# Optimization experiments

Measured on AMD Instinct MI355X. Metric: run time of the kernel, lower is better.

## Reference

```python
import jax, jax.numpy as jnp
import numpy as np

S = 4096
F = 512  # in_features, head_num == 1 so per-head dim == F


def setup_inputs() -> dict:
    key = jax.random.key(0)
    ks = jax.random.split(key, 11)
    std = 0.02
    inp = {
        "q": jax.random.normal(ks[0], (1, S, F), jnp.float32),
        "k": jax.random.normal(ks[1], (1, S, F), jnp.float32),
        "v": jax.random.normal(ks[2], (1, S, F), jnp.float32),
        "Wq": jax.random.normal(ks[3], (F, F), jnp.float32) * std,
        "bq": jax.random.normal(ks[4], (F,), jnp.float32) * std,
        "Wk": jax.random.normal(ks[5], (F, F), jnp.float32) * std,
        "bk": jax.random.normal(ks[6], (F,), jnp.float32) * std,
        "Wv": jax.random.normal(ks[7], (F, F), jnp.float32) * std,
        "bv": jax.random.normal(ks[8], (F,), jnp.float32) * std,
        "Wo": jax.random.normal(ks[9], (F, F), jnp.float32) * std,
        "bo": jax.random.normal(ks[10], (F,), jnp.float32) * std,
    }
    return inp


def reference(q, k, v, Wq, bq, Wk, bk, Wv, bv, Wo, bo):
    dk = Wq.shape[0]  # head_num == 1 -> per-head dim equals in_features
    # q_k, q_v: projections of q WITHOUT activation (as in original forward)
    q_k = q @ Wk.T + bk            # (1, S, F)
    q_v = q @ Wv.T + bv            # (1, S, F)
    # activated projections (F.relu)
    qq = jax.nn.relu(q @ Wq.T + bq)[0]  # (S, F)
    kk = jax.nn.relu(k @ Wk.T + bk)[0]  # (S, F)
    vv = jax.nn.relu(v @ Wv.T + bv)[0]  # (S, F)
    # diagonal of qq @ q_k^T, computed without materializing the SxS matrix
    q_att = jnp.sum(qq * q_k[0], axis=-1, keepdims=True)  # (S, 1)
    scores = jnp.einsum('sd,td->st', qq, kk)               # (S, S)
    scores = jnp.concatenate([scores, q_att], axis=-1)     # (S, S+1)
    scores = scores / np.sqrt(dk + 1).astype(np.float32)
    attn = jax.nn.softmax(scores, axis=-1)                 # (S, S+1)
    res = attn[:, :-1] @ vv                                # (S, F)
    res = q_v[0] * q_att + res                             # elementwise fusion
    y = res[None]                                          # (1, S, F)
    y = jax.nn.relu(y @ Wo.T + bo)
    return y
```

## Files before the change

### kernel.cpp

```cpp
#include <hip/hip_runtime.h>
#include <math.h>

#define S_LEN 4096
#define F_DIM 512
#define PSPLIT 8
#define FIXED_M 4.0f

typedef __attribute__((ext_vector_type(8))) short bf16x8;
typedef __attribute__((ext_vector_type(4))) float f32x4;

__device__ __forceinline__ unsigned short f2bf(float x) {
    union { float f; unsigned u; } v; v.f = x;
    unsigned r = v.u + 0x7fffu + ((v.u >> 16) & 1u);
    return (unsigned short)(r >> 16);
}
__device__ __forceinline__ float bf2f(unsigned short b) {
    union { unsigned u; float f; } v; v.u = ((unsigned)b) << 16;
    return v.f;
}
__device__ __forceinline__ void load_lds16(const void* g, void* l) {
    __builtin_amdgcn_global_load_lds(
        (const __attribute__((address_space(1))) unsigned int*)g,
        (__attribute__((address_space(3))) unsigned int*)l, 16, 0, 0);
}

struct CastArgs {
    const float* src[7];
    unsigned short* dst[7];
    int n4[7];
};
__global__ void cast_all(CastArgs a) {
    int r = blockIdx.y;
    int i = blockIdx.x * blockDim.x + threadIdx.x;
    if (i >= a.n4[r]) return;
    float4 v = ((const float4*)a.src[r])[i];
    ushort4 o;
    o.x = f2bf(v.x); o.y = f2bf(v.y); o.z = f2bf(v.z); o.w = f2bf(v.w);
    ((ushort4*)a.dst[r])[i] = o;
}

__global__ void transpose_bf16(const unsigned short* __restrict__ src,
                               unsigned short* __restrict__ dst) {
    __shared__ __align__(16) unsigned short tile[64][72];
    const int s0 = blockIdx.x * 64, f0 = blockIdx.y * 64;
    const int tid = threadIdx.x;
#pragma unroll
    for (int it = 0; it < 2; ++it) {
        int u = it * 256 + tid;
        int r = u >> 3, c = (u & 7) * 8;
        *(uint4*)&tile[r][c] = *(const uint4*)(src + (size_t)(s0 + r) * F_DIM + f0 + c);
    }
    __syncthreads();
#pragma unroll
    for (int it = 0; it < 2; ++it) {
        int u = it * 256 + tid;
        int fl = u >> 3, sc = (u & 7) * 8;
        unsigned short tmp[8];
#pragma unroll
        for (int i = 0; i < 8; ++i) tmp[i] = tile[sc + i][fl];
        *(uint4*)(dst + (size_t)(f0 + fl) * S_LEN + s0 + sc) = *(uint4*)tmp;
    }
}

#define GEMM_KLOOP(XPTR, LDX, WPTR, LDW, KBEG, KEND)                                  \
    for (int k0 = (KBEG); k0 < (KEND); k0 += 64) {                                    \
        __syncthreads();                                                              \
        _Pragma("unroll")                                                             \
        for (int i = 0; i < 2; ++i) {                                                 \
            int c = w * 2 + i;                                                        \
            _Pragma("unroll")                                                         \
            for (int kh = 0; kh < 2; ++kh) {                                          \
                load_lds16((XPTR) + (size_t)(m0 + c * 16 + ln) * (LDX) + k0 + kh * 32 + quad * 8, \
                           &As[(c * 2 + kh) * 512]);                                  \
                load_lds16((WPTR) + (size_t)(n0 + c * 16 + ln) * (LDW) + k0 + kh * 32 + quad * 8, \
                           &Bs[(c * 2 + kh) * 512]);                                  \
            }                                                                         \
        }                                                                             \
        __syncthreads();                                                              \
        _Pragma("unroll")                                                             \
        for (int kh = 0; kh < 2; ++kh) {                                              \
            bf16x8 af[4], bfr[4];                                                     \
            _Pragma("unroll")                                                         \
            for (int mt = 0; mt < 4; ++mt)                                            \
                af[mt] = *(const bf16x8*)&As[((wr * 4 + mt) * 2 + kh) * 512 + l * 8];  \
            _Pragma("unroll")                                                         \
            for (int nt = 0; nt < 4; ++nt)                                            \
                bfr[nt] = *(const bf16x8*)&Bs[((wc * 4 + nt) * 2 + kh) * 512 + l * 8]; \
            _Pragma("unroll")                                                         \
            for (int mt = 0; mt < 4; ++mt)                                            \
                _Pragma("unroll")                                                     \
                for (int nt = 0; nt < 4; ++nt)                                        \
                    acc[mt][nt] = __builtin_amdgcn_mfma_f32_16x16x32_bf16(            \
                        af[mt], bfr[nt], acc[mt][nt], 0, 0, 0);                       \
        }                                                                             \
    }

#define KLOOP256(XPTR, LDX, WPTR, LDW, KBEG, KEND)                                    \
    for (int k0 = (KBEG); k0 < (KEND); k0 += 64) {                                    \
        __syncthreads();                                                              \
        _Pragma("unroll")                                                             \
        for (int i = 0; i < 4; ++i) {                                                 \
            int g = w * 4 + i;                                                        \
            _Pragma("unroll")                                                         \
            for (int kh = 0; kh < 2; ++kh)                                            \
                load_lds16((XPTR) + (size_t)(m0 + g * 16 + ln) * (LDX) + k0 + kh * 32 + quad * 8, \
                           &As[(g * 2 + kh) * 512]);                                  \
        }                                                                             \
        _Pragma("unroll")                                                             \
        for (int i = 0; i < 2; ++i) {                                                 \
            int g2 = w * 2 + i;                                                       \
            _Pragma("unroll")                                                         \
            for (int kh = 0; kh < 2; ++kh)                                            \
                load_lds16((WPTR) + (size_t)(n0 + g2 * 16 + ln) * (LDW) + k0 + kh * 32 + quad * 8, \
                           &Bs[(g2 * 2 + kh) * 512]);                                 \
        }                                                                             \
        __syncthreads();                                                              \
        _Pragma("unroll")                                                             \
        for (int kh = 0; kh < 2; ++kh) {                                              \
            bf16x8 af[4], bfr[8];                                                     \
            _Pragma("unroll")                                                         \
            for (int mt = 0; mt < 4; ++mt)                                            \
                af[mt] = *(const bf16x8*)&As[((w * 4 + mt) * 2 + kh) * 512 + l * 8];   \
            _Pragma("unroll")                                                         \
            for (int nt = 0; nt < 8; ++nt)                                            \
                bfr[nt] = *(const bf16x8*)&Bs[(nt * 2 + kh) * 512 + l * 8];            \
            _Pragma("unroll")                                                         \
            for (int mt = 0; mt < 4; ++mt)                                            \
                _Pragma("unroll")                                                     \
                for (int nt = 0; nt < 8; ++nt)                                        \
                    acc[mt][nt] = __builtin_amdgcn_mfma_f32_16x16x32_bf16(            \
                        af[mt], bfr[nt], acc[mt][nt], 0, 0, 0);                       \
        }                                                                             \
    }

struct GemmDesc {
    const unsigned short* X;
    const unsigned short* W;
    const float* bias;
    unsigned short* out_bf;
    float* out_f32;
    int relu;
};
struct GemmArgs { GemmDesc d[5]; };

__launch_bounds__(256, 2)
__global__ void gemm128(GemmArgs args) {
    __shared__ __align__(16) unsigned short As[16 * 512];
    __shared__ __align__(16) unsigned short Bs[16 * 512];
    const GemmDesc d = args.d[blockIdx.y >> 2];
    const int n0 = (blockIdx.y & 3) * 128;
    const int m0 = blockIdx.x * 128;
    const int tid = threadIdx.x;
    const int w = tid >> 6, l = tid & 63, quad = l >> 4, ln = l & 15;
    const int wr = w >> 1, wc = w & 1;

    f32x4 acc[4][4];
    f32x4 zero4 = {0.f, 0.f, 0.f, 0.f};
#pragma unroll
    for (int i = 0; i < 4; ++i)
#pragma unroll
        for (int j = 0; j < 4; ++j) acc[i][j] = zero4;

    GEMM_KLOOP(d.X, F_DIM, d.W, F_DIM, 0, F_DIM)

#pragma unroll
    for (int mt = 0; mt < 4; ++mt)
#pragma unroll
        for (int nt = 0; nt < 4; ++nt)
#pragma unroll
            for (int r = 0; r < 4; ++r) {
                int row = m0 + wr * 64 + mt * 16 + quad * 4 + r;
                int col = n0 + wc * 64 + nt * 16 + ln;
                float vv = acc[mt][nt][r] + d.bias[col];
                if (d.relu) vv = fmaxf(vv, 0.f);
                if (d.out_bf)  d.out_bf[(size_t)row * F_DIM + col] = f2bf(vv);
                if (d.out_f32) d.out_f32[(size_t)row * F_DIM + col] = vv;
            }
}

__launch_bounds__(256, 2)
__global__ void gemm_exp(const unsigned short* __restrict__ X,
                         const unsigned short* __restrict__ W,
                         unsigned short* __restrict__ P,
                         float* __restrict__ lpart) {
    __shared__ __align__(16) unsigned short As[32 * 512];
    __shared__ __align__(16) unsigned short Bs[16 * 512];
    const float scale = 0.04415108f;
    const int nb = blockIdx.y;
    const int n0 = nb * 128;
    const int m0 = blockIdx.x * 256;
    const int tid = threadIdx.x;
    const int w = tid >> 6, l = tid & 63, quad = l >> 4, ln = l & 15;

    f32x4 acc[4][8];
    f32x4 zero4 = {0.f, 0.f, 0.f, 0.f};
#pragma unroll
    for (int i = 0; i < 4; ++i)
#pragma unroll
        for (int j = 0; j < 8; ++j) acc[i][j] = zero4;

    KLOOP256(X, F_DIM, W, F_DIM, 0, F_DIM)

#pragma unroll
    for (int mt = 0; mt < 4; ++mt)
#pragma unroll
        for (int r = 0; r < 4; ++r) {
            int row = m0 + w * 64 + mt * 16 + quad * 4 + r;
            float rs = 0.f;
#pragma unroll
            for (int nt = 0; nt < 8; ++nt) {
                int col = n0 + nt * 16 + ln;
                float p = __expf(acc[mt][nt][r] * scale - FIXED_M);
                P[(size_t)row * S_LEN + col] = f2bf(p);
                rs += p;
            }
            rs += __shfl_xor(rs, 1);
            rs += __shfl_xor(rs, 2);
            rs += __shfl_xor(rs, 4);
            rs += __shfl_xor(rs, 8);
            if (ln == 0) lpart[(size_t)nb * S_LEN + row] = rs;
        }
}

__launch_bounds__(256, 2)
__global__ void gemm_pv(const unsigned short* __restrict__ P,
                        const unsigned short* __restrict__ vt,
                        unsigned short* __restrict__ O_p) {
    __shared__ __align__(16) unsigned short As[32 * 512];
    __shared__ __align__(16) unsigned short Bs[16 * 512];
    const int nb = blockIdx.y & 3;
    const int split = blockIdx.y >> 2;
    const int n0 = nb * 128;
    const int m0 = blockIdx.x * 256;
    const int koff = split * (S_LEN / PSPLIT);
    const int tid = threadIdx.x;
    const int w = tid >> 6, l = tid & 63, quad = l >> 4, ln = l & 15;

    f32x4 acc[4][8];
    f32x4 zero4 = {0.f, 0.f, 0.f, 0.f};
#pragma unroll
    for (int i = 0; i < 4; ++i)
#pragma unroll
        for (int j = 0; j < 8; ++j) acc[i][j] = zero4;

    KLOOP256(P, S_LEN, vt, S_LEN, koff, koff + S_LEN / PSPLIT)

    unsigned short* Op = O_p + (size_t)split * S_LEN * F_DIM;
#pragma unroll
    for (int mt = 0; mt < 4; ++mt)
#pragma unroll
        for (int nt = 0; nt < 8; ++nt)
#pragma unroll
            for (int r = 0; r < 4; ++r) {
                int row = m0 + w * 64 + mt * 16 + quad * 4 + r;
                int col = n0 + nt * 16 + ln;
                Op[(size_t)row * F_DIM + col] = f2bf(acc[mt][nt][r]);
            }
}

__launch_bounds__(256, 2)
__global__ void gemm_final(const unsigned short* __restrict__ X,
                           const unsigned short* __restrict__ W,
                           float* __restrict__ Fp) {
    __shared__ __align__(16) unsigned short As[16 * 512];
    __shared__ __align__(16) unsigned short Bs[16 * 512];
    const int nb = blockIdx.y & 3;
    const int kseg = blockIdx.y >> 2;
    const int n0 = nb * 128;
    const int m0 = blockIdx.x * 128;
    const int tid = threadIdx.x;
    const int w = tid >> 6, l = tid & 63, quad = l >> 4, ln = l & 15;
    const int wr = w >> 1, wc = w & 1;

    f32x4 acc[4][4];
    f32x4 zero4 = {0.f, 0.f, 0.f, 0.f};
#pragma unroll
    for (int i = 0; i < 4; ++i)
#pragma unroll
        for (int j = 0; j < 4; ++j) acc[i][j] = zero4;

    GEMM_KLOOP(X, F_DIM, W, F_DIM, kseg * 256, kseg * 256 + 256)

    float* Op = Fp + (size_t)kseg * S_LEN * F_DIM;
#pragma unroll
    for (int mt = 0; mt < 4; ++mt)
#pragma unroll
        for (int nt = 0; nt < 4; ++nt)
#pragma unroll
            for (int r = 0; r < 4; ++r) {
                int row = m0 + wr * 64 + mt * 16 + quad * 4 + r;
                int col = n0 + wc * 64 + nt * 16 + ln;
                Op[(size_t)row * F_DIM + col] = acc[mt][nt][r];
            }
}

__global__ void reduce_final(const float* __restrict__ Fp,
                             const float* __restrict__ bias,
                             float* __restrict__ out) {
    int i = blockIdx.x * blockDim.x + threadIdx.x;
    int col4 = (i & (F_DIM / 4 - 1)) * 4;
    float4 a = ((const float4*)Fp)[i];
    float4 b = ((const float4*)(Fp + (size_t)S_LEN * F_DIM))[i];
    float4 bi = *(const float4*)(bias + col4);
    float4 o;
    o.x = fmaxf(a.x + b.x + bi.x, 0.f);
    o.y = fmaxf(a.y + b.y + bi.y, 0.f);
    o.z = fmaxf(a.z + b.z + bi.z, 0.f);
    o.w = fmaxf(a.w + b.w + bi.w, 0.f);
    ((float4*)out)[i] = o;
}

__global__ void combine_kernel(const unsigned short* __restrict__ O_p,
                               const float* __restrict__ lpart,
                               const unsigned short* __restrict__ qq,
                               const unsigned short* __restrict__ qk,
                               const unsigned short* __restrict__ qv,
                               unsigned short* __restrict__ res_bf) {
    const float scale = 0.04415108f;
    int row = blockIdx.x;
    int t = threadIdx.x;
    int wv = t >> 6, l = t & 63;
    __shared__ float wsum[2];

    ushort4 a = *(const ushort4*)(qq + (size_t)row * F_DIM + t * 4);
    ushort4 b = *(const ushort4*)(qk + (size_t)row * F_DIM + t * 4);
    float part = bf2f(a.x) * bf2f(b.x) + bf2f(a.y) * bf2f(b.y) +
                 bf2f(a.z) * bf2f(b.z) + bf2f(a.w) * bf2f(b.w);
#pragma unroll
    for (int off = 32; off >= 1; off >>= 1) part += __shfl_xor(part, off);
    if (l == 0) wsum[wv] = part;
    __syncthreads();
    float qa = wsum[0] + wsum[1];

    float denom = __expf(qa * scale - FIXED_M);
#pragma unroll
    for (int i = 0; i < 32; ++i) denom += lpart[(size_t)i * S_LEN + row];
    float inv = 1.f / denom;

    for (int f = t; f < F_DIM; f += 128) {
        float acc = 0.f;
#pragma unroll
        for (int i = 0; i < PSPLIT; ++i)
            acc += bf2f(O_p[((size_t)i * S_LEN + row) * F_DIM + f]);
        float r = bf2f(qv[(size_t)row * F_DIM + f]) * qa + acc * inv;
        res_bf[(size_t)row * F_DIM + f] = f2bf(r);
    }
}

extern "C" void kernel_launch(void* const* d_in, const int* in_sizes, int n_in,
                              void* d_out, int out_size, void* d_ws, size_t ws_size,
                              hipStream_t stream) {
    const float* q  = (const float*)d_in[0];
    const float* k  = (const float*)d_in[1];
    const float* v  = (const float*)d_in[2];
    const float* Wq = (const float*)d_in[3];
    const float* bq = (const float*)d_in[4];
    const float* Wk = (const float*)d_in[5];
    const float* bk = (const float*)d_in[6];
    const float* Wv = (const float*)d_in[7];
    const float* bv = (const float*)d_in[8];
    const float* Wo = (const float*)d_in[9];
    const float* bo = (const float*)d_in[10];
    float* out = (float*)d_out;

    char* p = (char*)d_ws;
    auto alloc = [&](size_t bytes) -> char* {
        char* r = p; p += (bytes + 255) & ~(size_t)255; return r;
    };
    const size_t SF = (size_t)S_LEN * F_DIM;
    unsigned short* q_bf  = (unsigned short*)alloc(SF * 2);
    unsigned short* k_bf  = (unsigned short*)alloc(SF * 2);
    unsigned short* v_bf  = (unsigned short*)alloc(SF * 2);
    unsigned short* qq_bf = (unsigned short*)alloc(SF * 2);
    unsigned short* kk_bf = (unsigned short*)alloc(SF * 2);
    unsigned short* vv_bf = (unsigned short*)alloc(SF * 2);
    unsigned short* vt_bf = (unsigned short*)alloc(SF * 2);
    unsigned short* qk_bf = (unsigned short*)alloc(SF * 2);
    unsigned short* qv_bf = (unsigned short*)alloc(SF * 2);
    unsigned short* res_bf = (unsigned short*)alloc(SF * 2);
    unsigned short* wq_bf = (unsigned short*)alloc((size_t)F_DIM * F_DIM * 2);
    unsigned short* wk_bf = (unsigned short*)alloc((size_t)F_DIM * F_DIM * 2);
    unsigned short* wv_bf = (unsigned short*)alloc((size_t)F_DIM * F_DIM * 2);
    unsigned short* wo_bf = (unsigned short*)alloc((size_t)F_DIM * F_DIM * 2);
    unsigned short* P_bf  = (unsigned short*)alloc((size_t)S_LEN * S_LEN * 2);
    float* lpart = (float*)alloc((size_t)32 * S_LEN * 4);
    unsigned short* O_p = (unsigned short*)alloc((size_t)PSPLIT * SF * 2);
    float* Fp = (float*)alloc((size_t)2 * SF * 4);

    CastArgs ca;
    ca.src[0] = q;  ca.dst[0] = q_bf;  ca.n4[0] = (int)(SF / 4);
    ca.src[1] = k;  ca.dst[1] = k_bf;  ca.n4[1] = (int)(SF / 4);
    ca.src[2] = v;  ca.dst[2] = v_bf;  ca.n4[2] = (int)(SF / 4);
    ca.src[3] = Wq; ca.dst[3] = wq_bf; ca.n4[3] = F_DIM * F_DIM / 4;
    ca.src[4] = Wk; ca.dst[4] = wk_bf; ca.n4[4] = F_DIM * F_DIM / 4;
    ca.src[5] = Wv; ca.dst[5] = wv_bf; ca.n4[5] = F_DIM * F_DIM / 4;
    ca.src[6] = Wo; ca.dst[6] = wo_bf; ca.n4[6] = F_DIM * F_DIM / 4;
    cast_all<<<dim3((unsigned)(SF / 4 / 256), 7), 256, 0, stream>>>(ca);

    GemmArgs ga;
    ga.d[0] = { q_bf, wq_bf, bq, qq_bf, nullptr, 1 };
    ga.d[1] = { k_bf, wk_bf, bk, kk_bf, nullptr, 1 };
    ga.d[2] = { v_bf, wv_bf, bv, vv_bf, nullptr, 1 };
    ga.d[3] = { q_bf, wk_bf, bk, qk_bf, nullptr, 0 };
    ga.d[4] = { q_bf, wv_bf, bv, qv_bf, nullptr, 0 };
    gemm128<<<dim3(S_LEN / 128, 20), 256, 0, stream>>>(ga);

    transpose_bf16<<<dim3(S_LEN / 64, F_DIM / 64), 256, 0, stream>>>(vv_bf, vt_bf);

    gemm_exp<<<dim3(S_LEN / 256, S_LEN / 128), 256, 0, stream>>>(qq_bf, kk_bf, P_bf, lpart);

    gemm_pv<<<dim3(S_LEN / 256, 4 * PSPLIT), 256, 0, stream>>>(P_bf, vt_bf, O_p);

    combine_kernel<<<S_LEN, 128, 0, stream>>>(O_p, lpart, qq_bf, qk_bf, qv_bf, res_bf);

    gemm_final<<<dim3(S_LEN / 128, 8), 256, 0, stream>>>(res_bf, wo_bf, Fp);
    reduce_final<<<(unsigned)(SF / 4 / 256), 256, 0, stream>>>(Fp, bo, out);
}
```

Measured before the change: 219.6 us.

## Double-buffer LDS tiles in all GEMM k-loops and halve PV split count

Replaces the single-buffered 64-wide k-loops with double-buffered 32-wide loops that prefetch the next k-slice into a second LDS buffer while MFMAs run on the current one. Each iteration then has one barrier instead of two. PSPLIT drops from 8 to 4, so the PV GEMM does longer k-loops and writes fewer partial outputs, at the cost of fewer blocks. The 128-tile kernels raise launch bounds to 3 blocks per CU. The risk is the single barrier per step: the prefetch is issued right after the barrier into the buffer other waves may still be reading, and the async LDS loads carry no explicit wait before use.

```diff
diff --git a/kernel.cpp b/kernel.cpp
--- a/kernel.cpp
+++ b/kernel.cpp
@@ -3,7 +3,7 @@
 
 #define S_LEN 4096
 #define F_DIM 512
-#define PSPLIT 8
+#define PSPLIT 4
 #define FIXED_M 4.0f
 
 typedef __attribute__((ext_vector_type(8))) short bf16x8;
@@ -62,30 +62,35 @@
     }
 }
 
-#define GEMM_KLOOP(XPTR, LDX, WPTR, LDW, KBEG, KEND)                                  \
-    for (int k0 = (KBEG); k0 < (KEND); k0 += 64) {                                    \
-        __syncthreads();                                                              \
+#define KLOOP128_DB(XPTR, LDX, WPTR, LDW, KBEG, KEND)                                 \
+    {                                                                                 \
+        const int nk = ((KEND) - (KBEG)) / 32;                                        \
         _Pragma("unroll")                                                             \
         for (int i = 0; i < 2; ++i) {                                                 \
             int c = w * 2 + i;                                                        \
-            _Pragma("unroll")                                                         \
-            for (int kh = 0; kh < 2; ++kh) {                                          \
-                load_lds16((XPTR) + (size_t)(m0 + c * 16 + ln) * (LDX) + k0 + kh * 32 + quad * 8, \
-                           &As[(c * 2 + kh) * 512]);                                  \
-                load_lds16((WPTR) + (size_t)(n0 + c * 16 + ln) * (LDW) + k0 + kh * 32 + quad * 8, \
-                           &Bs[(c * 2 + kh) * 512]);                                  \
+            load_lds16((XPTR) + (size_t)(m0 + c * 16 + ln) * (LDX) + (KBEG) + quad * 8, &As[c * 512]); \
+            load_lds16((WPTR) + (size_t)(n0 + c * 16 + ln) * (LDW) + (KBEG) + quad * 8, &Bs[c * 512]); \
+        }                                                                             \
+        for (int t = 0; t < nk; ++t) {                                                \
+            __syncthreads();                                                          \
+            const int cur = (t & 1) * 4096;                                           \
+            if (t + 1 < nk) {                                                         \
+                const int nxt = ((t + 1) & 1) * 4096;                                 \
+                const int k1 = (KBEG) + (t + 1) * 32;                                 \
+                _Pragma("unroll")                                                     \
+                for (int i = 0; i < 2; ++i) {                                         \
+                    int c = w * 2 + i;                                                \
+                    load_lds16((XPTR) + (size_t)(m0 + c * 16 + ln) * (LDX) + k1 + quad * 8, &As[nxt + c * 512]); \
+                    load_lds16((WPTR) + (size_t)(n0 + c * 16 + ln) * (LDW) + k1 + quad * 8, &Bs[nxt + c * 512]); \
+                }                                                                     \
             }                                                                         \
-        }                                                                             \
-        __syncthreads();                                                              \
-        _Pragma("unroll")                                                             \
-        for (int kh = 0; kh < 2; ++kh) {                                              \
             bf16x8 af[4], bfr[4];                                                     \
             _Pragma("unroll")                                                         \
             for (int mt = 0; mt < 4; ++mt)                                            \
-                af[mt] = *(const bf16x8*)&As[((wr * 4 + mt) * 2 + kh) * 512 + l * 8];  \
+                af[mt] = *(const bf16x8*)&As[cur + (wr * 4 + mt) * 512 + l * 8];      \
             _Pragma("unroll")                                                         \
             for (int nt = 0; nt < 4; ++nt)                                            \
-                bfr[nt] = *(const bf16x8*)&Bs[((wc * 4 + nt) * 2 + kh) * 512 + l * 8]; \
+                bfr[nt] = *(const bf16x8*)&Bs[cur + (wc * 4 + nt) * 512 + l * 8];     \
             _Pragma("unroll")                                                         \
             for (int mt = 0; mt < 4; ++mt)                                            \
                 _Pragma("unroll")                                                     \
@@ -95,35 +100,39 @@
         }                                                                             \
     }
 
-#define KLOOP256(XPTR, LDX, WPTR, LDW, KBEG, KEND)                                    \
-    for (int k0 = (KBEG); k0 < (KEND); k0 += 64) {                                    \
-        __syncthreads();                                                              \
+#define KLOOP256_DB(XPTR, LDX, WPTR, LDW, KBEG, KEND)                                 \
+    {                                                                                 \
+        const int nk = ((KEND) - (KBEG)) / 32;                                        \
         _Pragma("unroll")                                                             \
-        for (int i = 0; i < 4; ++i) {                                                 \
-            int g = w * 4 + i;                                                        \
-            _Pragma("unroll")                                                         \
-            for (int kh = 0; kh < 2; ++kh)                                            \
-                load_lds16((XPTR) + (size_t)(m0 + g * 16 + ln) * (LDX) + k0 + kh * 32 + quad * 8, \
-                           &As[(g * 2 + kh) * 512]);                                  \
-        }                                                                             \
+        for (int i = 0; i < 4; ++i)                                                   \
+            load_lds16((XPTR) + (size_t)(m0 + (w * 4 + i) * 16 + ln) * (LDX) + (KBEG) + quad * 8, \
+                       &As[(w * 4 + i) * 512]);                                       \
         _Pragma("unroll")                                                             \
-        for (int i = 0; i < 2; ++i) {                                                 \
-            int g2 = w * 2 + i;                                                       \
-            _Pragma("unroll")                                                         \
-            for (int kh = 0; kh < 2; ++kh)                                            \
-                load_lds16((WPTR) + (size_t)(n0 + g2 * 16 + ln) * (LDW) + k0 + kh * 32 + quad * 8, \
-                           &Bs[(g2 * 2 + kh) * 512]);                                 \
-        }                                                                             \
-        __syncthreads();                                                              \
-        _Pragma("unroll")                                                             \
-        for (int kh = 0; kh < 2; ++kh) {                                              \
+        for (int i = 0; i < 2; ++i)                                                   \
+            load_lds16((WPTR) + (size_t)(n0 + (w * 2 + i) * 16 + ln) * (LDW) + (KBEG) + quad * 8, \
+                       &Bs[(w * 2 + i) * 512]);                                       \
+        for (int t = 0; t < nk; ++t) {                                                \
+            __syncthreads();                                                          \
+            const int curA = (t & 1) * 8192, curB = (t & 1) * 4096;                   \
+            if (t + 1 < nk) {                                                         \
+                const int nxtA = ((t + 1) & 1) * 8192, nxtB = ((t + 1) & 1) * 4096;   \
+                const int k1 = (KBEG) + (t + 1) * 32;                                 \
+                _Pragma("unroll")                                                     \
+                for (int i = 0; i < 4; ++i)                                           \
+                    load_lds16((XPTR) + (size_t)(m0 + (w * 4 + i) * 16 + ln) * (LDX) + k1 + quad * 8, \
+                               &As[nxtA + (w * 4 + i) * 512]);                        \
+                _Pragma("unroll")                                                     \
+                for (int i = 0; i < 2; ++i)                                           \
+                    load_lds16((WPTR) + (size_t)(n0 + (w * 2 + i) * 16 + ln) * (LDW) + k1 + quad * 8, \
+                               &Bs[nxtB + (w * 2 + i) * 512]);                        \
+            }                                                                         \
             bf16x8 af[4], bfr[8];                                                     \
             _Pragma("unroll")                                                         \
             for (int mt = 0; mt < 4; ++mt)                                            \
-                af[mt] = *(const bf16x8*)&As[((w * 4 + mt) * 2 + kh) * 512 + l * 8];   \
+                af[mt] = *(const bf16x8*)&As[curA + (w * 4 + mt) * 512 + l * 8];      \
             _Pragma("unroll")                                                         \
             for (int nt = 0; nt < 8; ++nt)                                            \
-                bfr[nt] = *(const bf16x8*)&Bs[(nt * 2 + kh) * 512 + l * 8];            \
+                bfr[nt] = *(const bf16x8*)&Bs[curB + nt * 512 + l * 8];               \
             _Pragma("unroll")                                                         \
             for (int mt = 0; mt < 4; ++mt)                                            \
                 _Pragma("unroll")                                                     \
@@ -143,10 +152,10 @@
 };
 struct GemmArgs { GemmDesc d[5]; };
 
-__launch_bounds__(256, 2)
+__launch_bounds__(256, 3)
 __global__ void gemm128(GemmArgs args) {
-    __shared__ __align__(16) unsigned short As[16 * 512];
-    __shared__ __align__(16) unsigned short Bs[16 * 512];
+    __shared__ __align__(16) unsigned short As[2 * 8 * 512];
+    __shared__ __align__(16) unsigned short Bs[2 * 8 * 512];
     const GemmDesc d = args.d[blockIdx.y >> 2];
     const int n0 = (blockIdx.y & 3) * 128;
     const int m0 = blockIdx.x * 128;
@@ -161,7 +170,7 @@
 #pragma unroll
         for (int j = 0; j < 4; ++j) acc[i][j] = zero4;
 
-    GEMM_KLOOP(d.X, F_DIM, d.W, F_DIM, 0, F_DIM)
+    KLOOP128_DB(d.X, F_DIM, d.W, F_DIM, 0, F_DIM)
 
 #pragma unroll
     for (int mt = 0; mt < 4; ++mt)
@@ -183,8 +192,8 @@
                          const unsigned short* __restrict__ W,
                          unsigned short* __restrict__ P,
                          float* __restrict__ lpart) {
-    __shared__ __align__(16) unsigned short As[32 * 512];
-    __shared__ __align__(16) unsigned short Bs[16 * 512];
+    __shared__ __align__(16) unsigned short As[2 * 16 * 512];
+    __shared__ __align__(16) unsigned short Bs[2 * 8 * 512];
     const float scale = 0.04415108f;
     const int nb = blockIdx.y;
     const int n0 = nb * 128;
@@ -199,7 +208,7 @@
 #pragma unroll
         for (int j = 0; j < 8; ++j) acc[i][j] = zero4;
 
-    KLOOP256(X, F_DIM, W, F_DIM, 0, F_DIM)
+    KLOOP256_DB(X, F_DIM, W, F_DIM, 0, F_DIM)
 
 #pragma unroll
     for (int mt = 0; mt < 4; ++mt)
@@ -226,8 +235,8 @@
 __global__ void gemm_pv(const unsigned short* __restrict__ P,
                         const unsigned short* __restrict__ vt,
                         unsigned short* __restrict__ O_p) {
-    __shared__ __align__(16) unsigned short As[32 * 512];
-    __shared__ __align__(16) unsigned short Bs[16 * 512];
+    __shared__ __align__(16) unsigned short As[2 * 16 * 512];
+    __shared__ __align__(16) unsigned short Bs[2 * 8 * 512];
     const int nb = blockIdx.y & 3;
     const int split = blockIdx.y >> 2;
     const int n0 = nb * 128;
@@ -243,7 +252,7 @@
 #pragma unroll
         for (int j = 0; j < 8; ++j) acc[i][j] = zero4;
 
-    KLOOP256(P, S_LEN, vt, S_LEN, koff, koff + S_LEN / PSPLIT)
+    KLOOP256_DB(P, S_LEN, vt, S_LEN, koff, koff + S_LEN / PSPLIT)
 
     unsigned short* Op = O_p + (size_t)split * S_LEN * F_DIM;
 #pragma unroll
@@ -258,12 +267,12 @@
             }
 }
 
-__launch_bounds__(256, 2)
+__launch_bounds__(256, 3)
 __global__ void gemm_final(const unsigned short* __restrict__ X,
                            const unsigned short* __restrict__ W,
                            float* __restrict__ Fp) {
-    __shared__ __align__(16) unsigned short As[16 * 512];
-    __shared__ __align__(16) unsigned short Bs[16 * 512];
+    __shared__ __align__(16) unsigned short As[2 * 8 * 512];
+    __shared__ __align__(16) unsigned short Bs[2 * 8 * 512];
     const int nb = blockIdx.y & 3;
     const int kseg = blockIdx.y >> 2;
     const int n0 = nb * 128;
@@ -279,7 +288,7 @@
 #pragma unroll
         for (int j = 0; j < 4; ++j) acc[i][j] = zero4;
 
-    GEMM_KLOOP(X, F_DIM, W, F_DIM, kseg * 256, kseg * 256 + 256)
+    KLOOP128_DB(X, F_DIM, W, F_DIM, kseg * 256, kseg * 256 + 256)
 
     float* Op = Fp + (size_t)kseg * S_LEN * F_DIM;
 #pragma unroll
```

After: 240.7 us. 1.1x slower.
